# Optimization experiments

Measured on AMD Instinct MI355X. Metric: run time of the kernel, lower is better.

Reference implementation:

```python
import jax, jax.numpy as jnp
import numpy as np

K_NEIGHBORS = 16
IGNORE_INDEX = -1
LOSS_WEIGHT = 1.0
N_POINTS = 262144
NUM_CLASSES = 20


def setup_inputs() -> dict:
    key = jax.random.key(0)
    k1, k2, k3, k4 = jax.random.split(key, 4)
    seg_logits = jax.random.normal(k1, (N_POINTS, NUM_CLASSES), dtype=jnp.float32)
    coord = jax.random.normal(k2, (N_POINTS, 3), dtype=jnp.float32)
    labels = jax.random.randint(k3, (N_POINTS,), 0, NUM_CLASSES, dtype=jnp.int64)
    # KNN indices are computed under no_grad in the original (pointops.knn_query);
    # here they are synthetic in-range indices (no -1 padding entries).
    reference_index = jax.random.randint(k4, (N_POINTS, K_NEIGHBORS), 0, N_POINTS, dtype=jnp.int64)
    return {
        "seg_logits": seg_logits,
        "coord": coord,
        "labels": labels,
        "reference_index": reference_index,
    }


def reference(seg_logits, coord, labels, reference_index):
    # coord is only used by the (no-grad) KNN query in the original; indices are given.
    probs = jax.nn.softmax(seg_logits, axis=1)              # [N, C]
    idx = jnp.maximum(reference_index, 0)                   # safe gather index
    knn_mask = reference_index >= 0                         # sign(idx+1).bool()
    neighbor_labels = labels[idx]                           # [N, k]
    same_label_mask = labels[:, None] == neighbor_labels
    center_valid = (labels != IGNORE_INDEX)[:, None]
    neighbor_valid = neighbor_labels != IGNORE_INDEX
    total_mask = knn_mask & center_valid & neighbor_valid & same_label_mask  # [N, k]

    neighbor_probs = probs[idx]                             # [N, k, C]
    prob_dist_sq = jnp.sum((probs[:, None, :] - neighbor_probs) ** 2, axis=2)  # [N, k]
    sum_loss = jnp.sum(prob_dist_sq * total_mask.astype(probs.dtype))
    num_valid = jnp.maximum(jnp.sum(total_mask).astype(probs.dtype), 1.0)
    return (sum_loss / num_valid) * LOSS_WEIGHT
```

## Files before the change

kernel.cpp:

```cpp
#include <hip/hip_runtime.h>

#define NCLS 20
#define IGNORE_INDEX (-1)
#define TPB 1024
#define PAIRS_PER_THREAD 8
#define PPB (TPB * PAIRS_PER_THREAD)
#define HASH_WORDS 16384

__device__ __forceinline__ void softmax_row(const float* __restrict__ row, float* v) {
    const float4* r4 = (const float4*)row;
#pragma unroll
    for (int q = 0; q < 5; ++q) {
        float4 t = r4[q];
        v[4 * q + 0] = t.x; v[4 * q + 1] = t.y;
        v[4 * q + 2] = t.z; v[4 * q + 3] = t.w;
    }
    float mx = v[0];
#pragma unroll
    for (int c = 1; c < NCLS; ++c) mx = fmaxf(mx, v[c]);
    float s = 0.f;
#pragma unroll
    for (int c = 0; c < NCLS; ++c) { v[c] = __expf(v[c] - mx); s += v[c]; }
    float inv = 1.0f / s;
#pragma unroll
    for (int c = 0; c < NCLS; ++c) v[c] *= inv;
}

__global__ __launch_bounds__(256) void hash_prep(const int* __restrict__ labels,
                                                 unsigned int* __restrict__ H,
                                                 int words) {
    int w = blockIdx.x * blockDim.x + threadIdx.x;
    if (w >= words) return;
    const int4* lp = (const int4*)(labels + (size_t)w * 16);
    int4 v0 = lp[0], v1 = lp[1], v2 = lp[2], v3 = lp[3];
    int l[16] = {v0.x, v0.y, v0.z, v0.w, v1.x, v1.y, v1.z, v1.w,
                 v2.x, v2.y, v2.z, v2.w, v3.x, v3.y, v3.z, v3.w};
    unsigned int acc = 0;
#pragma unroll
    for (int k = 0; k < 16; ++k)
        acc |= ((unsigned int)(l[k] & 3)) << (2 * k);
    H[w] = acc;
}

__global__ __launch_bounds__(TPB) void fused_kernel(
    const float* __restrict__ logits, const int* __restrict__ labels,
    const int* __restrict__ ref_idx, const unsigned int* __restrict__ H,
    unsigned int* __restrict__ counts, float* __restrict__ partials,
    long long total_pairs) {
    __shared__ unsigned int s_hash[HASH_WORDS];
    const int tid = threadIdx.x;

    {
        const uint4* src = (const uint4*)H;
        uint4* dst = (uint4*)s_hash;
#pragma unroll
        for (int i = 0; i < 4; ++i) dst[tid + i * TPB] = src[tid + i * TPB];
    }
    __syncthreads();

    float fsum = 0.f;
    unsigned int cnt = 0;
    const long long pair0 = (long long)blockIdx.x * PPB +
                            (long long)tid * PAIRS_PER_THREAD;
    if (pair0 + PAIRS_PER_THREAD <= total_pairs) {
        const int p = (int)(pair0 >> 4);
        const int li = labels[p];
        int4 ra = *(const int4*)(ref_idx + pair0);
        int4 rb = *(const int4*)(ref_idx + pair0 + 4);
        int rr[8] = {ra.x, ra.y, ra.z, ra.w, rb.x, rb.y, rb.z, rb.w};
        if (li != IGNORE_INDEX) {
            const unsigned int h_li = (unsigned int)(li & 3);
            unsigned int hv[8];
#pragma unroll
            for (int j = 0; j < 8; ++j) {
                int idx = max(rr[j], 0);
                hv[j] = (s_hash[idx >> 4] >> (2 * (idx & 15))) & 3u;
            }
#pragma unroll
            for (int j = 0; j < 8; ++j) {
                if (rr[j] >= 0 && hv[j] == h_li) {
                    int nl = labels[rr[j]];
                    if (nl == li) {
                        float a[NCLS], b[NCLS];
                        softmax_row(logits + (size_t)p * NCLS, a);
                        softmax_row(logits + (size_t)rr[j] * NCLS, b);
                        float d = 0.f;
#pragma unroll
                        for (int k = 0; k < NCLS; ++k) {
                            float dx = a[k] - b[k];
                            d = fmaf(dx, dx, d);
                        }
                        fsum += d;
                        cnt += 1u;
                    }
                }
            }
        }
    }

#pragma unroll
    for (int off = 32; off > 0; off >>= 1) {
        fsum += __shfl_down(fsum, off, 64);
        cnt  += __shfl_down(cnt,  off, 64);
    }
    __syncthreads();
    float* s_f        = (float*)s_hash;
    unsigned int* s_c = s_hash + 64;
    if ((tid & 63) == 0) { s_f[tid >> 6] = fsum; s_c[tid >> 6] = cnt; }
    __syncthreads();
    if (tid == 0) {
        float ts = 0.f; unsigned int tc = 0;
#pragma unroll
        for (int w = 0; w < TPB / 64; ++w) { ts += s_f[w]; tc += s_c[w]; }
        partials[blockIdx.x] = ts;
        counts[blockIdx.x] = tc;
    }
}

__global__ __launch_bounds__(1024) void reduce_kernel(
    const float* __restrict__ partials, const unsigned int* __restrict__ counts,
    float* __restrict__ out, int m) {
    double dsum = 0.0;
    unsigned long long cnt = 0;
    for (int i = threadIdx.x; i < m; i += 1024) {
        dsum += (double)partials[i];
        cnt  += (unsigned long long)min(counts[i], (unsigned int)PPB);
    }
#pragma unroll
    for (int off = 32; off > 0; off >>= 1) {
        dsum += __shfl_down(dsum, off, 64);
        cnt  += __shfl_down(cnt,  off, 64);
    }
    __shared__ double s_sum[16];
    __shared__ unsigned long long s_cnt[16];
    const int wave = threadIdx.x >> 6;
    if ((threadIdx.x & 63) == 0) { s_sum[wave] = dsum; s_cnt[wave] = cnt; }
    __syncthreads();
    if (threadIdx.x == 0) {
        double ts = 0.0; unsigned long long tc = 0;
        for (int w = 0; w < 16; ++w) { ts += s_sum[w]; tc += s_cnt[w]; }
        if (tc < 1ull) tc = 1ull;
        out[0] = (float)(ts / (double)tc);
    }
}

extern "C" void kernel_launch(void* const* d_in, const int* in_sizes, int n_in,
                              void* d_out, int out_size, void* d_ws, size_t ws_size,
                              hipStream_t stream) {
    const float* seg_logits = (const float*)d_in[0];
    const int* labels  = (const int*)d_in[2];
    const int* ref_idx = (const int*)d_in[3];
    float* out = (float*)d_out;
    const int n = in_sizes[2];
    const long long total_pairs = (long long)n * 16;
    const int blocks = (int)((total_pairs + PPB - 1) / PPB);

    unsigned int* H        = (unsigned int*)d_ws;
    unsigned int* counts   = (unsigned int*)((char*)d_ws + HASH_WORDS * 4);
    float* partials        = (float*)((char*)d_ws + HASH_WORDS * 4 + 512 * 4);

    hash_prep<<<(HASH_WORDS + 255) / 256, 256, 0, stream>>>(labels, H, HASH_WORDS);
    fused_kernel<<<blocks, TPB, 0, stream>>>(seg_logits, labels, ref_idx, H,
                                             counts, partials, total_pairs);
    reduce_kernel<<<1, 1024, 0, stream>>>(partials, counts, out, blocks);
}
```

Baseline: 123.4 us.

## Compact hash-surviving pairs into shared buffer to remove warp divergence

Instead of each thread computing the label check and softmax distance inline for its candidate pairs, which diverges within a wave, candidates that pass the 2-bit hash filter are appended to a shared-memory queue via an atomic counter. After a barrier, all threads drain the queue densely, doing the label check and distance computation. The goal is to keep the sparse surviving pairs, about 1/4 from the hash filter and about 1/20 after the label match, on full waves. It adds shared atomics, an extra barrier and extra shared memory; any overflow past the buffer capacity falls back to inline work.

```diff
diff --git a/kernel.cpp b/kernel.cpp
--- a/kernel.cpp
+++ b/kernel.cpp
@@ -6,6 +6,8 @@
 #define PAIRS_PER_THREAD 8
 #define PPB (TPB * PAIRS_PER_THREAD)
 #define HASH_WORDS 16384
+#define BUFCAP 1024
+#define RBITS 18
 
 __device__ __forceinline__ void softmax_row(const float* __restrict__ row, float* v) {
     const float4* r4 = (const float4*)row;
@@ -24,6 +26,20 @@
     float inv = 1.0f / s;
 #pragma unroll
     for (int c = 0; c < NCLS; ++c) v[c] *= inv;
+}
+
+__device__ __forceinline__ float pair_dist(const float* __restrict__ logits,
+                                           int p, int r) {
+    float a[NCLS], b[NCLS];
+    softmax_row(logits + (size_t)p * NCLS, a);
+    softmax_row(logits + (size_t)r * NCLS, b);
+    float d = 0.f;
+#pragma unroll
+    for (int k = 0; k < NCLS; ++k) {
+        float dx = a[k] - b[k];
+        d = fmaf(dx, dx, d);
+    }
+    return d;
 }
 
 __global__ __launch_bounds__(256) void hash_prep(const int* __restrict__ labels,
@@ -48,7 +64,12 @@
     unsigned int* __restrict__ counts, float* __restrict__ partials,
     long long total_pairs) {
     __shared__ unsigned int s_hash[HASH_WORDS];
+    __shared__ uint2 s_buf[BUFCAP];
+    __shared__ int s_cnt;
+    __shared__ float s_wsum[TPB / 64];
+    __shared__ unsigned int s_wcnt[TPB / 64];
     const int tid = threadIdx.x;
+    if (tid == 0) s_cnt = 0;
 
     {
         const uint4* src = (const uint4*)H;
@@ -60,6 +81,7 @@
 
     float fsum = 0.f;
     unsigned int cnt = 0;
+
     const long long pair0 = (long long)blockIdx.x * PPB +
                             (long long)tid * PAIRS_PER_THREAD;
     if (pair0 + PAIRS_PER_THREAD <= total_pairs) {
@@ -79,22 +101,31 @@
 #pragma unroll
             for (int j = 0; j < 8; ++j) {
                 if (rr[j] >= 0 && hv[j] == h_li) {
-                    int nl = labels[rr[j]];
-                    if (nl == li) {
-                        float a[NCLS], b[NCLS];
-                        softmax_row(logits + (size_t)p * NCLS, a);
-                        softmax_row(logits + (size_t)rr[j] * NCLS, b);
-                        float d = 0.f;
-#pragma unroll
-                        for (int k = 0; k < NCLS; ++k) {
-                            float dx = a[k] - b[k];
-                            d = fmaf(dx, dx, d);
-                        }
-                        fsum += d;
-                        cnt += 1u;
+                    int slot = atomicAdd(&s_cnt, 1);
+                    if (slot < BUFCAP) {
+                        s_buf[slot] = make_uint2(
+                            ((unsigned int)li << RBITS) | (unsigned int)rr[j],
+                            (unsigned int)p);
+                    } else {
+                        int nl = labels[rr[j]];
+                        if (nl == li) { fsum += pair_dist(logits, p, rr[j]); cnt += 1u; }
                     }
                 }
             }
+        }
+    }
+    __syncthreads();
+    const int c = min(s_cnt, BUFCAP);
+
+    for (int i = tid; i < c; i += TPB) {
+        uint2 e = s_buf[i];
+        int r  = (int)(e.x & ((1u << RBITS) - 1u));
+        int li = (int)(e.x >> RBITS);
+        int p  = (int)e.y;
+        int nl = labels[r];
+        if (nl == li) {
+            fsum += pair_dist(logits, p, r);
+            cnt += 1u;
         }
     }
 
@@ -103,15 +134,12 @@
         fsum += __shfl_down(fsum, off, 64);
         cnt  += __shfl_down(cnt,  off, 64);
     }
-    __syncthreads();
-    float* s_f        = (float*)s_hash;
-    unsigned int* s_c = s_hash + 64;
-    if ((tid & 63) == 0) { s_f[tid >> 6] = fsum; s_c[tid >> 6] = cnt; }
+    if ((tid & 63) == 0) { s_wsum[tid >> 6] = fsum; s_wcnt[tid >> 6] = cnt; }
     __syncthreads();
     if (tid == 0) {
         float ts = 0.f; unsigned int tc = 0;
 #pragma unroll
-        for (int w = 0; w < TPB / 64; ++w) { ts += s_f[w]; tc += s_c[w]; }
+        for (int w = 0; w < TPB / 64; ++w) { ts += s_wsum[w]; tc += s_wcnt[w]; }
         partials[blockIdx.x] = ts;
         counts[blockIdx.x] = tc;
     }
@@ -155,9 +183,9 @@
     const long long total_pairs = (long long)n * 16;
     const int blocks = (int)((total_pairs + PPB - 1) / PPB);
 
-    unsigned int* H        = (unsigned int*)d_ws;
-    unsigned int* counts   = (unsigned int*)((char*)d_ws + HASH_WORDS * 4);
-    float* partials        = (float*)((char*)d_ws + HASH_WORDS * 4 + 512 * 4);
+    unsigned int* H      = (unsigned int*)d_ws;
+    unsigned int* counts = (unsigned int*)((char*)d_ws + HASH_WORDS * 4);
+    float* partials      = (float*)((char*)d_ws + HASH_WORDS * 4 + 512 * 4);
 
     hash_prep<<<(HASH_WORDS + 255) / 256, 256, 0, stream>>>(labels, H, HASH_WORDS);
     fused_kernel<<<blocks, TPB, 0, stream>>>(seg_logits, labels, ref_idx, H,
```

New measurement: 118.8 us. -3.8%, faster.
